# Kernel optimization log

Measured on AMD Instinct MI355X. Metric: run time of the kernel, lower is better.

The kernel has to match this reference:

```python
import jax, jax.numpy as jnp
import numpy as np

N_NODES = 50000
N_EDGES = 800000
IN_C, HID_C, OUT_C = 256, 256, 128


def setup_inputs() -> dict:
    key = jax.random.key(0)
    k1, k2, k3, k4 = jax.random.split(key, 4)
    x = jax.random.normal(k1, (N_NODES, IN_C), dtype=jnp.float32)
    edge_index = jax.random.randint(k2, (2, N_EDGES), 0, N_NODES, dtype=jnp.int64)
    W1 = jax.random.normal(k3, (IN_C, HID_C), dtype=jnp.float32) / np.sqrt(IN_C)
    b1 = jnp.zeros((HID_C,), dtype=jnp.float32)
    W2 = jax.random.normal(k4, (HID_C, OUT_C), dtype=jnp.float32) / np.sqrt(HID_C)
    b2 = jnp.zeros((OUT_C,), dtype=jnp.float32)
    return {"x": x, "edge_index": edge_index, "W1": W1, "b1": b1, "W2": W2, "b2": b2}


def _gcn_norm(edge_index, n_nodes):
    # Add self-loops, compute symmetric normalization D^-1/2 (A+I) D^-1/2 (PyG GCNConv default).
    loop = jnp.arange(n_nodes, dtype=edge_index.dtype)
    src = jnp.concatenate([edge_index[0], loop])  # [E+N]
    dst = jnp.concatenate([edge_index[1], loop])  # [E+N]
    deg = jax.ops.segment_sum(jnp.ones_like(dst, dtype=jnp.float32), dst, num_segments=n_nodes)
    dinv = jnp.where(deg > 0, 1.0 / jnp.sqrt(deg), 0.0)
    norm = dinv[src] * dinv[dst]  # [E+N]
    return src, dst, norm


def _gcn_conv(x, src, dst, norm, W, b, n_nodes):
    h = x @ W                                  # [N, out] dense GEMM first (PyG order)
    msg = h[src] * norm[:, None]               # gather + scale: [E+N, out]
    out = jax.ops.segment_sum(msg, dst, num_segments=n_nodes)  # scatter-add
    return out + b


def reference(x, edge_index, W1, b1, W2, b2):
    n = x.shape[0]
    src, dst, norm = _gcn_norm(edge_index, n)
    h = _gcn_conv(x, src, dst, norm, W1, b1, n)
    h = jax.nn.relu(h)
    # dropout is identity in eval mode
    return _gcn_conv(h, src, dst, norm, W2, b2, n)
```

## Files before the change

kernel.cpp:

```cpp
#include <hip/hip_runtime.h>
#include <cstdint>
#include <cstddef>


static constexpr int CH1 = 256;
static constexpr int CH2 = 128;

typedef __attribute__((ext_vector_type(8))) short bf16x8;
typedef __attribute__((ext_vector_type(4))) float f32x4;
typedef __attribute__((ext_vector_type(8))) unsigned short u16x8;

__device__ inline unsigned short f2bf(float f) {
  unsigned u = __builtin_bit_cast(unsigned, f);
  return (unsigned short)((u + 0x7fffu + ((u >> 16) & 1u)) >> 16);
}

__device__ inline void gload16(const void* g, void* l) {
  __builtin_amdgcn_global_load_lds(
      (const __attribute__((address_space(1))) unsigned int*)g,
      (__attribute__((address_space(3))) unsigned int*)l, 16, 0, 0);
}


__global__ void k_init_deg(int* __restrict__ deg, int n, int* __restrict__ flag) {
  int i = blockIdx.x * blockDim.x + threadIdx.x;
  if (i < n) deg[i] = 0;
  if (i == 0) *flag = 0;
}

__global__ void k_detect_i32(const unsigned int* __restrict__ w, int nwords,
                             int* __restrict__ flag) {
  int i = blockIdx.x * blockDim.x + threadIdx.x;
  if (i < nwords && (i & 1) && w[i] != 0u) *flag = 1;
}

__global__ void k_cvt_deg(const void* __restrict__ raw, int* __restrict__ e32,
                          int* __restrict__ deg, int E, const int* __restrict__ flag) {
  int i = blockIdx.x * blockDim.x + threadIdx.x;
  if (i >= 2 * E) return;
  int v = (*flag) ? ((const int*)raw)[i] : (int)((const long long*)raw)[i];
  e32[i] = v;
  if (i >= E) atomicAdd(&deg[v], 1);
}

__global__ __launch_bounds__(256) void k_chunk_sum(const int* __restrict__ deg,
                                                   int* __restrict__ bsum, int N) {
  __shared__ int sh[256];
  int i = blockIdx.x * 256 + threadIdx.x;
  sh[threadIdx.x] = (i < N) ? deg[i] : 0;
  __syncthreads();
  for (int off = 128; off > 0; off >>= 1) {
    if (threadIdx.x < (unsigned)off) sh[threadIdx.x] += sh[threadIdx.x + off];
    __syncthreads();
  }
  if (threadIdx.x == 0) bsum[blockIdx.x] = sh[0];
}

__global__ __launch_bounds__(256) void k_scan_bsums(int* __restrict__ bsum, int nb) {
  __shared__ int sh[256];
  int t = threadIdx.x;
  int v = (t < nb) ? bsum[t] : 0;
  sh[t] = v;
  __syncthreads();
  for (int off = 1; off < 256; off <<= 1) {
    int add = (t >= off) ? sh[t - off] : 0;
    __syncthreads();
    sh[t] += add;
    __syncthreads();
  }
  if (t < nb) bsum[t] = sh[t] - v;
}

__global__ __launch_bounds__(256) void k_chunk_scan(
    const int* __restrict__ deg, const int* __restrict__ bsum,
    int* __restrict__ rowstart, int* __restrict__ cursor,
    float* __restrict__ dinv, int N, int E) {
  __shared__ int sh[256];
  int t = threadIdx.x;
  int i = blockIdx.x * 256 + t;
  int d = (i < N) ? deg[i] : 0;
  sh[t] = d;
  __syncthreads();
  for (int off = 1; off < 256; off <<= 1) {
    int add = (t >= off) ? sh[t - off] : 0;
    __syncthreads();
    sh[t] += add;
    __syncthreads();
  }
  if (i < N) {
    int rs = bsum[blockIdx.x] + sh[t] - d;
    rowstart[i] = rs;
    cursor[i]   = rs;
    dinv[i] = rsqrtf((float)(d + 1));
  }
  if (i == 0) rowstart[N] = E;
}

__global__ void k_fill(const int* __restrict__ src, const int* __restrict__ dst,
                       int* __restrict__ cursor, int* __restrict__ csr, int E) {
  int e = blockIdx.x * blockDim.x + threadIdx.x;
  if (e < E) {
    int pos = atomicAdd(&cursor[dst[e]], 1);
    csr[pos] = src[e];
  }
}

__global__ void k_prep(const float4* __restrict__ x, u16x8* __restrict__ xo, int n8x,
                       const float* __restrict__ W1, unsigned short* __restrict__ w1t,
                       int Ka, int Na,
                       const float* __restrict__ W2, unsigned short* __restrict__ w2t,
                       int Kb, int Nb) {
  int i = blockIdx.x * blockDim.x + threadIdx.x;
  if (i < n8x) {
    float4 a = x[i * 2], b = x[i * 2 + 1];
    u16x8 p;
    p[0] = f2bf(a.x); p[1] = f2bf(a.y); p[2] = f2bf(a.z); p[3] = f2bf(a.w);
    p[4] = f2bf(b.x); p[5] = f2bf(b.y); p[6] = f2bf(b.z); p[7] = f2bf(b.w);
    xo[i] = p;
    return;
  }
  i -= n8x;
  if (i < Ka * Na) {
    int k = i / Na, n = i - k * Na;
    w1t[(size_t)n * Ka + k] = f2bf(W1[i]);
    return;
  }
  i -= Ka * Na;
  if (i < Kb * Nb) {
    int k = i / Nb, n = i - k * Nb;
    w2t[(size_t)n * Kb + k] = f2bf(W2[i]);
  }
}

template <int BN>
__global__ __launch_bounds__(512) void k_gemm_mfma(
    const unsigned short* __restrict__ A, const unsigned short* __restrict__ Bt,
    const float* __restrict__ dinv, unsigned short* __restrict__ Co, int M, int K) {
  constexpr int BM = 128, BK = 32;
  constexpr int NF = BN / 64;
  constexpr int ASZ = BM * BK;
  constexpr int BSZ = BN * BK;
  __shared__ unsigned short lds[2][ASZ + BSZ];
  const int t = threadIdx.x;
  const int w = t >> 6, l = t & 63;
  const int wm = w >> 2, wn = w & 3;
  const int m0 = blockIdx.x * BM;
  const int lr = l & 15, lk = l >> 4;

  auto stage = [&](int buf, int k0) {
    unsigned short* base = lds[buf];
    {
      int row = t >> 2, p = t & 3;
      int s = p ^ ((row >> 1) & 3);
      int gm = m0 + row; if (gm >= M) gm = M - 1;
      gload16(A + (size_t)gm * K + k0 + s * 8, base + (size_t)row * BK + p * 8);
    }
    for (int i = t; i < BN * 4; i += 512) {
      int n = i >> 2, p = i & 3;
      int s = p ^ ((n >> 1) & 3);
      gload16(Bt + (size_t)n * K + k0 + s * 8, base + ASZ + (size_t)n * BK + p * 8);
    }
  };

  f32x4 acc[4][NF];
#pragma unroll
  for (int a = 0; a < 4; ++a)
#pragma unroll
    for (int b = 0; b < NF; ++b) acc[a][b] = (f32x4){0.f, 0.f, 0.f, 0.f};

  stage(0, 0);
  __syncthreads();
  const int nsteps = K / BK;
  for (int ks = 0; ks < nsteps; ++ks) {
    int cur = ks & 1;
    if (ks + 1 < nsteps) stage(cur ^ 1, (ks + 1) * BK);
    const unsigned short* base = lds[cur];
    bf16x8 ah[4], bh[NF];
#pragma unroll
    for (int fm = 0; fm < 4; ++fm) {
      int row = wm * 64 + fm * 16 + lr;
      int p = lk ^ ((row >> 1) & 3);
      ah[fm] = *(const bf16x8*)(base + row * BK + p * 8);
    }
#pragma unroll
    for (int fb = 0; fb < NF; ++fb) {
      int n = wn * (BN / 4) + fb * 16 + lr;
      int p = lk ^ ((n >> 1) & 3);
      bh[fb] = *(const bf16x8*)(base + ASZ + n * BK + p * 8);
    }
#pragma unroll
    for (int fm = 0; fm < 4; ++fm)
#pragma unroll
      for (int fb = 0; fb < NF; ++fb)
        acc[fm][fb] = __builtin_amdgcn_mfma_f32_16x16x32_bf16(ah[fm], bh[fb], acc[fm][fb], 0, 0, 0);
    __syncthreads();
  }
#pragma unroll
  for (int fm = 0; fm < 4; ++fm)
#pragma unroll
    for (int r = 0; r < 4; ++r) {
      int row = m0 + wm * 64 + fm * 16 + lk * 4 + r;
      if (row < M) {
        float dv = dinv[row];
#pragma unroll
        for (int fb = 0; fb < NF; ++fb) {
          int col = wn * (BN / 4) + fb * 16 + lr;
          size_t o = ((size_t)(col >> 6) * M + row) * 64 + (col & 63);
          Co[o] = f2bf(dv * acc[fm][fb][r]);
        }
      }
    }
}

template <int C, int MODE>
__global__ __launch_bounds__(256) void k_agg_slice(
    const int* __restrict__ rowstart, const int* __restrict__ csr,
    const float* __restrict__ dinv, const unsigned short* __restrict__ gS,
    const float* __restrict__ bias, float* __restrict__ out,
    unsigned short* __restrict__ of1, int N, int nodeblocks) {
  constexpr int NSL = C / 64;
  constexpr int DUP = 8 / NSL;
  const int x = blockIdx.x & 7;
  const int slice = x & (NSL - 1);
  const int dup = x >> (NSL == 4 ? 2 : 1);
  const int bstride = ((int)gridDim.x >> 3) * DUP;
  const int ln = threadIdx.x & 31;
  const int sub = ln >> 3;
  const int l8 = ln & 7;
  const unsigned short* __restrict__ base = gS + (size_t)slice * N * 64 + l8 * 8;
  const int c0 = slice * 64 + l8 * 8;
  const float4 bA = *(const float4*)(bias + c0);
  const float4 bB = *(const float4*)(bias + c0 + 4);

  const unsigned selL = 0x00003f80u;
  const unsigned selH = 0x3f800000u;
#define DOT2(k, word, sel) \
  asm("v_dot2_f32_bf16 %0, %1, %2, %0" : "+v"(acc[k]) : "v"(word), "v"(sel));
#define ACC8(u)                 \
  { DOT2(0, (u).x, selL) DOT2(1, (u).x, selH)  \
    DOT2(2, (u).y, selL) DOT2(3, (u).y, selH)  \
    DOT2(4, (u).z, selL) DOT2(5, (u).z, selH)  \
    DOT2(6, (u).w, selL) DOT2(7, (u).w, selH) }

  for (int nb = ((int)blockIdx.x >> 3) * DUP + dup; nb < nodeblocks; nb += bstride) {
    const int v = nb * 8 + ((int)threadIdx.x >> 5);
    if (v >= N) continue;
    float acc[8] = {0.f, 0.f, 0.f, 0.f, 0.f, 0.f, 0.f, 0.f};
    const int end = rowstart[v + 1];
    int j = rowstart[v] + sub;
    for (; j + 4 < end; j += 8) {
      int s0 = csr[j], s1 = csr[j + 4];
      uint4 r0 = *(const uint4*)(base + (size_t)s0 * 64);
      uint4 r1 = *(const uint4*)(base + (size_t)s1 * 64);
      ACC8(r0) ACC8(r1)
    }
    if (j < end) {
      uint4 r = *(const uint4*)(base + (size_t)csr[j] * 64);
      ACC8(r)
    }
#pragma unroll
    for (int k = 0; k < 8; ++k) {
      acc[k] += __shfl_xor(acc[k], 8, 32);
      acc[k] += __shfl_xor(acc[k], 16, 32);
    }
    if (sub == 0) {
      {
        uint4 r = *(const uint4*)(base + (size_t)v * 64);
        ACC8(r)
      }
      const float dv = dinv[v];
      float o[8];
      o[0] = dv * acc[0] + bA.x; o[1] = dv * acc[1] + bA.y;
      o[2] = dv * acc[2] + bA.z; o[3] = dv * acc[3] + bA.w;
      o[4] = dv * acc[4] + bB.x; o[5] = dv * acc[5] + bB.y;
      o[6] = dv * acc[6] + bB.z; o[7] = dv * acc[7] + bB.w;
      if constexpr (MODE == 1) {
        u16x8 p;
#pragma unroll
        for (int k = 0; k < 8; ++k) p[k] = f2bf(fmaxf(o[k], 0.f));
        *(u16x8*)(of1 + (size_t)v * C + c0) = p;
      } else {
        *(float4*)(out + (size_t)v * C + c0) = make_float4(o[0], o[1], o[2], o[3]);
        *(float4*)(out + (size_t)v * C + c0 + 4) = make_float4(o[4], o[5], o[6], o[7]);
      }
    }
  }
#undef ACC8
#undef DOT2
}


extern "C" void kernel_launch(void* const* d_in, const int* in_sizes, int n_in,
                              void* d_out, int out_size, void* d_ws, size_t ws_size,
                              hipStream_t stream) {
  const float* x  = (const float*)d_in[0];
  const void*  ei = d_in[1];
  const float* W1 = (const float*)d_in[2];
  const float* b1 = (const float*)d_in[3];
  const float* W2 = (const float*)d_in[4];
  const float* b2 = (const float*)d_in[5];
  float* out = (float*)d_out;

  const int N = in_sizes[0] / CH1;
  const int E = in_sizes[1] / 2;

  char* w = (char*)d_ws;
  size_t off = 0;
  auto alloc = [&](size_t bytes) -> void* {
    void* p = w + off;
    off += (bytes + 255) & ~(size_t)255;
    return p;
  };
  int*   deg      = (int*)alloc((size_t)N * 4);
  int*   flag     = (int*)alloc(256);
  int*   e32      = (int*)alloc((size_t)2 * E * 4);
  int*   rowstart = (int*)alloc((size_t)(N + 1) * 4);
  int*   cursor   = (int*)alloc((size_t)N * 4);
  int*   bsum     = (int*)alloc(256 * 4);
  int*   csr      = (int*)alloc((size_t)E * 4);
  float* dinv     = (float*)alloc((size_t)N * 4);
  unsigned short* xh  = (unsigned short*)alloc((size_t)N * CH1 * 2);
  unsigned short* g1S = (unsigned short*)alloc((size_t)N * CH1 * 2);
  unsigned short* g2S = (unsigned short*)alloc((size_t)N * CH2 * 2);
  unsigned short* w1t = (unsigned short*)alloc((size_t)CH1 * CH1 * 2);
  unsigned short* w2t = (unsigned short*)alloc((size_t)CH1 * CH2 * 2);

  const int* srcI = e32;
  const int* dstI = e32 + E;

  dim3 blk(256), blk512(512);
  auto cdiv = [](long long a, long long b) { return (int)((a + b - 1) / b); };
  const int nchunks = cdiv(N, 256);
  const int nodeblocks = cdiv(N, 8);
  const int n8x = N * CH1 / 8;
  const int AGG_GRID = 2048;

  k_init_deg<<<cdiv(N, 256), blk, 0, stream>>>(deg, N, flag);
  k_detect_i32<<<cdiv(2LL * E, 256), blk, 0, stream>>>((const unsigned int*)ei, 2 * E, flag);
  k_cvt_deg<<<cdiv(2LL * E, 256), blk, 0, stream>>>(ei, e32, deg, E, flag);
  k_chunk_sum<<<nchunks, blk, 0, stream>>>(deg, bsum, N);
  k_scan_bsums<<<1, blk, 0, stream>>>(bsum, nchunks);
  k_chunk_scan<<<nchunks, blk, 0, stream>>>(deg, bsum, rowstart, cursor, dinv, N, E);
  k_fill<<<cdiv(E, 256), blk, 0, stream>>>(srcI, dstI, cursor, csr, E);

  k_prep<<<cdiv((long long)n8x + CH1 * CH1 + CH1 * CH2, 256), blk, 0, stream>>>(
      (const float4*)x, (u16x8*)xh, n8x, W1, w1t, CH1, CH1, W2, w2t, CH1, CH2);

  k_gemm_mfma<CH1><<<cdiv(N, 128), blk512, 0, stream>>>(xh, w1t, dinv, g1S, N, CH1);
  k_agg_slice<CH1, 1><<<AGG_GRID, blk, 0, stream>>>(
      rowstart, csr, dinv, g1S, b1, nullptr, xh, N, nodeblocks);

  k_gemm_mfma<CH2><<<cdiv(N, 128), blk512, 0, stream>>>(xh, w2t, dinv, g2S, N, CH1);
  k_agg_slice<CH2, 0><<<AGG_GRID, blk, 0, stream>>>(
      rowstart, csr, dinv, g2S, b2, out, nullptr, N, nodeblocks);
}
```

Baseline: 225.9 us.

## Replace CSR prefix scan with atomic row allocation and fold init into prep

Drops the three-kernel prefix scan that built CSR row offsets. Each node instead grabs its segment through an atomicAdd on a global counter, and start/end pairs are stored as int2. Degree and flag initialisation is merged into the bf16 conversion kernel, and the int32 detection pass now reads only the high words. This removes several small launches. The cost is that row segments are no longer in node order, which may reduce locality of csr reads in aggregation, and the single global counter is heavily contended.

Result: no change. 226.0 us (+0.0%).

```diff
diff --git a/kernel.cpp b/kernel.cpp
--- a/kernel.cpp
+++ b/kernel.cpp
@@ -21,17 +21,41 @@
       (__attribute__((address_space(3))) unsigned int*)l, 16, 0, 0);
 }
 
-
-__global__ void k_init_deg(int* __restrict__ deg, int n, int* __restrict__ flag) {
+__global__ void k_prep(const float4* __restrict__ x, u16x8* __restrict__ xo, int n8x,
+                       const float* __restrict__ W1, unsigned short* __restrict__ w1t,
+                       int Ka, int Na,
+                       const float* __restrict__ W2, unsigned short* __restrict__ w2t,
+                       int Kb, int Nb,
+                       int* __restrict__ deg, int N,
+                       int* __restrict__ flag, int* __restrict__ gcnt) {
   int i = blockIdx.x * blockDim.x + threadIdx.x;
-  if (i < n) deg[i] = 0;
-  if (i == 0) *flag = 0;
-}
-
-__global__ void k_detect_i32(const unsigned int* __restrict__ w, int nwords,
+  if (i == 0) { *flag = 0; *gcnt = 0; }
+  if (i < N) deg[i] = 0;
+  if (i < n8x) {
+    float4 a = x[i * 2], b = x[i * 2 + 1];
+    u16x8 p;
+    p[0] = f2bf(a.x); p[1] = f2bf(a.y); p[2] = f2bf(a.z); p[3] = f2bf(a.w);
+    p[4] = f2bf(b.x); p[5] = f2bf(b.y); p[6] = f2bf(b.z); p[7] = f2bf(b.w);
+    xo[i] = p;
+    return;
+  }
+  int j = i - n8x;
+  if (j < Ka * Na) {
+    int k = j / Na, n = j - k * Na;
+    w1t[(size_t)n * Ka + k] = f2bf(W1[j]);
+    return;
+  }
+  j -= Ka * Na;
+  if (j < Kb * Nb) {
+    int k = j / Nb, n = j - k * Nb;
+    w2t[(size_t)n * Kb + k] = f2bf(W2[j]);
+  }
+}
+
+__global__ void k_detect_i32(const unsigned int* __restrict__ w, int E,
                              int* __restrict__ flag) {
   int i = blockIdx.x * blockDim.x + threadIdx.x;
-  if (i < nwords && (i & 1) && w[i] != 0u) *flag = 1;
+  if (i < E && w[2 * i + 1] != 0u) *flag = 1;
 }
 
 __global__ void k_cvt_deg(const void* __restrict__ raw, int* __restrict__ e32,
@@ -43,57 +67,16 @@
   if (i >= E) atomicAdd(&deg[v], 1);
 }
 
-__global__ __launch_bounds__(256) void k_chunk_sum(const int* __restrict__ deg,
-                                                   int* __restrict__ bsum, int N) {
-  __shared__ int sh[256];
-  int i = blockIdx.x * 256 + threadIdx.x;
-  sh[threadIdx.x] = (i < N) ? deg[i] : 0;
-  __syncthreads();
-  for (int off = 128; off > 0; off >>= 1) {
-    if (threadIdx.x < (unsigned)off) sh[threadIdx.x] += sh[threadIdx.x + off];
-    __syncthreads();
-  }
-  if (threadIdx.x == 0) bsum[blockIdx.x] = sh[0];
-}
-
-__global__ __launch_bounds__(256) void k_scan_bsums(int* __restrict__ bsum, int nb) {
-  __shared__ int sh[256];
-  int t = threadIdx.x;
-  int v = (t < nb) ? bsum[t] : 0;
-  sh[t] = v;
-  __syncthreads();
-  for (int off = 1; off < 256; off <<= 1) {
-    int add = (t >= off) ? sh[t - off] : 0;
-    __syncthreads();
-    sh[t] += add;
-    __syncthreads();
-  }
-  if (t < nb) bsum[t] = sh[t] - v;
-}
-
-__global__ __launch_bounds__(256) void k_chunk_scan(
-    const int* __restrict__ deg, const int* __restrict__ bsum,
-    int* __restrict__ rowstart, int* __restrict__ cursor,
-    float* __restrict__ dinv, int N, int E) {
-  __shared__ int sh[256];
-  int t = threadIdx.x;
-  int i = blockIdx.x * 256 + t;
-  int d = (i < N) ? deg[i] : 0;
-  sh[t] = d;
-  __syncthreads();
-  for (int off = 1; off < 256; off <<= 1) {
-    int add = (t >= off) ? sh[t - off] : 0;
-    __syncthreads();
-    sh[t] += add;
-    __syncthreads();
-  }
-  if (i < N) {
-    int rs = bsum[blockIdx.x] + sh[t] - d;
-    rowstart[i] = rs;
-    cursor[i]   = rs;
-    dinv[i] = rsqrtf((float)(d + 1));
-  }
-  if (i == 0) rowstart[N] = E;
+__global__ void k_alloc(const int* __restrict__ deg, int2* __restrict__ rowse,
+                        int* __restrict__ cursor, float* __restrict__ dinv,
+                        int* __restrict__ gcnt, int N) {
+  int v = blockIdx.x * blockDim.x + threadIdx.x;
+  if (v >= N) return;
+  int d = deg[v];
+  int rs = atomicAdd(gcnt, d);
+  rowse[v] = make_int2(rs, rs + d);
+  cursor[v] = rs;
+  dinv[v] = rsqrtf((float)(d + 1));
 }
 
 __global__ void k_fill(const int* __restrict__ src, const int* __restrict__ dst,
@@ -102,33 +85,6 @@
   if (e < E) {
     int pos = atomicAdd(&cursor[dst[e]], 1);
     csr[pos] = src[e];
-  }
-}
-
-__global__ void k_prep(const float4* __restrict__ x, u16x8* __restrict__ xo, int n8x,
-                       const float* __restrict__ W1, unsigned short* __restrict__ w1t,
-                       int Ka, int Na,
-                       const float* __restrict__ W2, unsigned short* __restrict__ w2t,
-                       int Kb, int Nb) {
-  int i = blockIdx.x * blockDim.x + threadIdx.x;
-  if (i < n8x) {
-    float4 a = x[i * 2], b = x[i * 2 + 1];
-    u16x8 p;
-    p[0] = f2bf(a.x); p[1] = f2bf(a.y); p[2] = f2bf(a.z); p[3] = f2bf(a.w);
-    p[4] = f2bf(b.x); p[5] = f2bf(b.y); p[6] = f2bf(b.z); p[7] = f2bf(b.w);
-    xo[i] = p;
-    return;
-  }
-  i -= n8x;
-  if (i < Ka * Na) {
-    int k = i / Na, n = i - k * Na;
-    w1t[(size_t)n * Ka + k] = f2bf(W1[i]);
-    return;
-  }
-  i -= Ka * Na;
-  if (i < Kb * Nb) {
-    int k = i / Nb, n = i - k * Nb;
-    w2t[(size_t)n * Kb + k] = f2bf(W2[i]);
   }
 }
 
@@ -214,7 +170,7 @@
 
 template <int C, int MODE>
 __global__ __launch_bounds__(256) void k_agg_slice(
-    const int* __restrict__ rowstart, const int* __restrict__ csr,
+    const int2* __restrict__ rowse, const int* __restrict__ csr,
     const float* __restrict__ dinv, const unsigned short* __restrict__ gS,
     const float* __restrict__ bias, float* __restrict__ out,
     unsigned short* __restrict__ of1, int N, int nodeblocks) {
@@ -246,8 +202,9 @@
     const int v = nb * 8 + ((int)threadIdx.x >> 5);
     if (v >= N) continue;
     float acc[8] = {0.f, 0.f, 0.f, 0.f, 0.f, 0.f, 0.f, 0.f};
-    const int end = rowstart[v + 1];
-    int j = rowstart[v] + sub;
+    const int2 se = rowse[v];
+    const int end = se.y;
+    int j = se.x + sub;
     for (; j + 4 < end; j += 8) {
       int s0 = csr[j], s1 = csr[j + 4];
       uint4 r0 = *(const uint4*)(base + (size_t)s0 * 64);
@@ -314,9 +271,8 @@
   int*   deg      = (int*)alloc((size_t)N * 4);
   int*   flag     = (int*)alloc(256);
   int*   e32      = (int*)alloc((size_t)2 * E * 4);
-  int*   rowstart = (int*)alloc((size_t)(N + 1) * 4);
+  int2*  rowse    = (int2*)alloc((size_t)N * 8);
   int*   cursor   = (int*)alloc((size_t)N * 4);
-  int*   bsum     = (int*)alloc(256 * 4);
   int*   csr      = (int*)alloc((size_t)E * 4);
   float* dinv     = (float*)alloc((size_t)N * 4);
   unsigned short* xh  = (unsigned short*)alloc((size_t)N * CH1 * 2);
@@ -324,33 +280,31 @@
   unsigned short* g2S = (unsigned short*)alloc((size_t)N * CH2 * 2);
   unsigned short* w1t = (unsigned short*)alloc((size_t)CH1 * CH1 * 2);
   unsigned short* w2t = (unsigned short*)alloc((size_t)CH1 * CH2 * 2);
+  int* gcnt = flag + 1;
 
   const int* srcI = e32;
   const int* dstI = e32 + E;
 
   dim3 blk(256), blk512(512);
   auto cdiv = [](long long a, long long b) { return (int)((a + b - 1) / b); };
-  const int nchunks = cdiv(N, 256);
   const int nodeblocks = cdiv(N, 8);
   const int n8x = N * CH1 / 8;
   const int AGG_GRID = 2048;
 
-  k_init_deg<<<cdiv(N, 256), blk, 0, stream>>>(deg, N, flag);
-  k_detect_i32<<<cdiv(2LL * E, 256), blk, 0, stream>>>((const unsigned int*)ei, 2 * E, flag);
+  k_prep<<<cdiv((long long)n8x + CH1 * CH1 + CH1 * CH2, 256), blk, 0, stream>>>(
+      (const float4*)x, (u16x8*)xh, n8x, W1, w1t, CH1, CH1, W2, w2t, CH1, CH2,
+      deg, N, flag, gcnt);
+
+  k_detect_i32<<<cdiv(E, 256), blk, 0, stream>>>((const unsigned int*)ei, E, flag);
   k_cvt_deg<<<cdiv(2LL * E, 256), blk, 0, stream>>>(ei, e32, deg, E, flag);
-  k_chunk_sum<<<nchunks, blk, 0, stream>>>(deg, bsum, N);
-  k_scan_bsums<<<1, blk, 0, stream>>>(bsum, nchunks);
-  k_chunk_scan<<<nchunks, blk, 0, stream>>>(deg, bsum, rowstart, cursor, dinv, N, E);
+  k_alloc<<<cdiv(N, 256), blk, 0, stream>>>(deg, rowse, cursor, dinv, gcnt, N);
   k_fill<<<cdiv(E, 256), blk, 0, stream>>>(srcI, dstI, cursor, csr, E);
-
-  k_prep<<<cdiv((long long)n8x + CH1 * CH1 + CH1 * CH2, 256), blk, 0, stream>>>(
-      (const float4*)x, (u16x8*)xh, n8x, W1, w1t, CH1, CH1, W2, w2t, CH1, CH2);
 
   k_gemm_mfma<CH1><<<cdiv(N, 128), blk512, 0, stream>>>(xh, w1t, dinv, g1S, N, CH1);
   k_agg_slice<CH1, 1><<<AGG_GRID, blk, 0, stream>>>(
-      rowstart, csr, dinv, g1S, b1, nullptr, xh, N, nodeblocks);
+      rowse, csr, dinv, g1S, b1, nullptr, xh, N, nodeblocks);
 
   k_gemm_mfma<CH2><<<cdiv(N, 128), blk512, 0, stream>>>(xh, w2t, dinv, g2S, N, CH1);
   k_agg_slice<CH2, 0><<<AGG_GRID, blk, 0, stream>>>(
-      rowstart, csr, dinv, g2S, b2, out, nullptr, N, nodeblocks);
-}
+      rowse, csr, dinv, g2S, b2, out, nullptr, N, nodeblocks);
+}
```
